# Optimization experiments

Hardware: AMD Instinct MI355X
Metric: run time of the kernel (lower is better)

The kernel has to match this reference:

```python
import jax, jax.numpy as jnp
import numpy as np

EPS = 1e-8  # torch.nn.functional.cosine_similarity default eps


def setup_inputs() -> dict:
    key = jax.random.key(0)
    k1, k2 = jax.random.split(key)
    P, B, D = 64, 512, 1024
    z_list = jax.random.normal(k1, (P, B, D), dtype=jnp.float32)
    z_avg = jax.random.normal(k2, (B, D), dtype=jnp.float32)  # passed but unused (overwritten in forward)
    return {"z_list": z_list, "z_avg": z_avg}


def reference(z_list, z_avg):
    # z_list: (P, B, D). The original overwrites z_avg with the patch mean.
    P, B, _ = z_list.shape
    z_avg = jnp.mean(z_list, axis=0)  # (B, D)

    # cosine_similarity(z_list[p,i], z_avg[j]) via normalize + batched matmul
    zn = z_list / jnp.maximum(jnp.linalg.norm(z_list, axis=-1, keepdims=True), EPS)
    an = z_avg / jnp.maximum(jnp.linalg.norm(z_avg, axis=-1, keepdims=True), EPS)
    cos_sim = jnp.einsum("pbd,cd->pbc", zn, an) - 1.0  # (P, B, B)

    mask = ~jnp.eye(B, dtype=bool)  # zero out diagonal (i == j)
    z_dissim = jnp.sum(cos_sim * mask[None, :, :])
    count = jnp.sum(mask) * P  # B*(B-1)*P
    return z_dissim / count
```

## Files before the change

kernel.cpp:

```cpp
#include <hip/hip_runtime.h>
#include <math.h>

constexpr int P = 64, B = 512, D = 1024;
constexpr int D4 = D / 4;
constexpr int WAVES = 4;
constexpr int PC = P / WAVES;
constexpr int TB = 32;
#define EPS 1e-8f

__device__ inline float wave_reduce_sum(float v) {
#pragma unroll
  for (int off = 1; off < 64; off <<= 1) v += __shfl_xor(v, off);
  return v;
}

__device__ inline float dot4(const float4& a, const float4& b) {
  return a.x * b.x + a.y * b.y + a.z * b.z + a.w * b.w;
}

__global__ __launch_bounds__(256) void k_main(const float* __restrict__ z,
                                              float* __restrict__ an,
                                              float* __restrict__ Uv,
                                              float* __restrict__ diag,
                                              float* __restrict__ out) {
  const int b = blockIdx.x;
  const int t = threadIdx.x;
  const int w = t >> 6;
  const int lane = t & 63;

  if (b == 0 && t == 0) out[0] = 0.f;

  __shared__ float4 lds_zs[WAVES][D4];
  __shared__ float4 lds_uu[WAVES][D4];
  __shared__ float red[2 * WAVES];

  float4 zs[4], uu[4];
#pragma unroll
  for (int k = 0; k < 4; ++k) {
    zs[k] = make_float4(0.f, 0.f, 0.f, 0.f);
    uu[k] = make_float4(0.f, 0.f, 0.f, 0.f);
  }

  const size_t pstride = (size_t)B * D4;
  const float4* base = (const float4*)z + ((size_t)(w * PC) * B + b) * D4;

  float4 curA[4], curB[4];
#pragma unroll
  for (int k = 0; k < 4; ++k) {
    curA[k] = base[k * 64 + lane];
    curB[k] = base[pstride + k * 64 + lane];
  }

  for (int pr = 0; pr < PC / 2; ++pr) {
    float4 nxtA[4], nxtB[4];
    const bool more = (pr + 1 < PC / 2);
    if (more) {
      const float4* nA = base + (size_t)(2 * pr + 2) * pstride;
      const float4* nB = base + (size_t)(2 * pr + 3) * pstride;
#pragma unroll
      for (int k = 0; k < 4; ++k) {
        nxtA[k] = nA[k * 64 + lane];
        nxtB[k] = nB[k * 64 + lane];
      }
    }

    float ssA = 0.f, ssB = 0.f;
#pragma unroll
    for (int k = 0; k < 4; ++k) {
      ssA += dot4(curA[k], curA[k]);
      ssB += dot4(curB[k], curB[k]);
    }
#pragma unroll
    for (int off = 1; off < 64; off <<= 1) {
      ssA += __shfl_xor(ssA, off);
      ssB += __shfl_xor(ssB, off);
    }
    const float wA = 1.0f / fmaxf(sqrtf(ssA), EPS);
    const float wB = 1.0f / fmaxf(sqrtf(ssB), EPS);

#pragma unroll
    for (int k = 0; k < 4; ++k) {
      zs[k].x += curA[k].x + curB[k].x;
      zs[k].y += curA[k].y + curB[k].y;
      zs[k].z += curA[k].z + curB[k].z;
      zs[k].w += curA[k].w + curB[k].w;
      uu[k].x += wA * curA[k].x + wB * curB[k].x;
      uu[k].y += wA * curA[k].y + wB * curB[k].y;
      uu[k].z += wA * curA[k].z + wB * curB[k].z;
      uu[k].w += wA * curA[k].w + wB * curB[k].w;
    }
    if (more) {
#pragma unroll
      for (int k = 0; k < 4; ++k) {
        curA[k] = nxtA[k];
        curB[k] = nxtB[k];
      }
    }
  }

#pragma unroll
  for (int k = 0; k < 4; ++k) {
    lds_zs[w][k * 64 + lane] = zs[k];
    lds_uu[w][k * 64 + lane] = uu[k];
  }
  __syncthreads();

  float4 zsum = make_float4(0.f, 0.f, 0.f, 0.f);
  float4 usum = make_float4(0.f, 0.f, 0.f, 0.f);
#pragma unroll
  for (int ww = 0; ww < WAVES; ++ww) {
    float4 a = lds_zs[ww][t];
    float4 u = lds_uu[ww][t];
    zsum.x += a.x; zsum.y += a.y; zsum.z += a.z; zsum.w += a.w;
    usum.x += u.x; usum.y += u.y; usum.z += u.z; usum.w += u.w;
  }

  float ss = dot4(zsum, zsum);
  ss = wave_reduce_sum(ss);
  if (lane == 0) red[w] = ss;
  __syncthreads();
  ss = red[0] + red[1] + red[2] + red[3];

  const float inv = 1.0f / fmaxf(sqrtf(ss), (float)P * EPS);
  float4 a4 = make_float4(zsum.x * inv, zsum.y * inv, zsum.z * inv, zsum.w * inv);

  ((float4*)an)[(size_t)b * D4 + t] = a4;
  ((float4*)Uv)[(size_t)b * D4 + t] = usum;

  float dg = dot4(usum, a4);
  dg = wave_reduce_sum(dg);
  if (lane == 0) red[WAVES + w] = dg;
  __syncthreads();
  if (t == 0) diag[b] = red[WAVES] + red[WAVES + 1] + red[WAVES + 2] + red[WAVES + 3];
}

__global__ __launch_bounds__(256) void k_tail(const float* __restrict__ an,
                                              const float* __restrict__ Uv,
                                              const float* __restrict__ diag,
                                              float* __restrict__ out) {
  const int blk = blockIdx.x;
  const int t = threadIdx.x;
  const int w = t >> 6;
  const int lane = t & 63;
  const int f4c = blk * 8 + (t & 7);
  const int rg = t >> 3;

  float4 S = make_float4(0.f, 0.f, 0.f, 0.f);
  float4 T = make_float4(0.f, 0.f, 0.f, 0.f);
#pragma unroll 4
  for (int i = 0; i < 16; ++i) {
    const size_t r = (size_t)rg + 32 * i;
    float4 a = ((const float4*)an)[r * D4 + f4c];
    float4 u = ((const float4*)Uv)[r * D4 + f4c];
    S.x += a.x; S.y += a.y; S.z += a.z; S.w += a.w;
    T.x += u.x; T.y += u.y; T.z += u.z; T.w += u.w;
  }

#pragma unroll
  for (int off = 8; off < 64; off <<= 1) {
    S.x += __shfl_xor(S.x, off); S.y += __shfl_xor(S.y, off);
    S.z += __shfl_xor(S.z, off); S.w += __shfl_xor(S.w, off);
    T.x += __shfl_xor(T.x, off); T.y += __shfl_xor(T.y, off);
    T.z += __shfl_xor(T.z, off); T.w += __shfl_xor(T.w, off);
  }

  __shared__ float4 ldsS[4][8], ldsT[4][8];
  if (lane < 8) {
    ldsS[w][lane] = S;
    ldsT[w][lane] = T;
  }
  __syncthreads();

  float dotp = 0.f;
  if (t < 8) {
    float4 Sf = ldsS[0][t], Tf = ldsT[0][t];
#pragma unroll
    for (int ww = 1; ww < 4; ++ww) {
      float4 s2 = ldsS[ww][t], t2 = ldsT[ww][t];
      Sf.x += s2.x; Sf.y += s2.y; Sf.z += s2.z; Sf.w += s2.w;
      Tf.x += t2.x; Tf.y += t2.y; Tf.z += t2.z; Tf.w += t2.w;
    }
    dotp = dot4(Sf, Tf);
  }
  float dgp = 0.f;
  if (t >= 16 && t < 32) dgp = diag[blk * 16 + (t - 16)];

  if (w == 0) {
    float v = dotp - dgp;
#pragma unroll
    for (int off = 1; off < 32; off <<= 1) v += __shfl_xor(v, off);
    if (t == 0) {
      const float count = 64.0f * 512.0f * 511.0f;
      float contrib = v / count + (blk == 0 ? -1.0f : 0.0f);
      atomicAdd(out, contrib);
    }
  }
}

extern "C" void kernel_launch(void* const* d_in, const int* in_sizes, int n_in,
                              void* d_out, int out_size, void* d_ws, size_t ws_size,
                              hipStream_t stream) {
  const float* z = (const float*)d_in[0];

  float* ws = (float*)d_ws;
  float* an = ws;
  float* Uv = an + (size_t)B * D;
  float* diag = Uv + (size_t)B * D;

  k_main<<<B, 256, 0, stream>>>(z, an, Uv, diag, (float*)d_out);
  k_tail<<<TB, 256, 0, stream>>>(an, Uv, diag, (float*)d_out);
}
```

Measured before the change: 31.97 us.

## Process two batch rows per block with contiguous 8 KB loads per patch

Each k_main block now handles two adjacent batch rows, so every patch step reads one contiguous 8 KB span (two rows) instead of two separate rows from different patches. The grid is halved to 256 blocks, and each thread keeps accumulators for both rows, which doubles register use. The goal is better memory coalescing and fewer blocks. In exchange, fewer blocks means fewer waves in flight to hide DRAM latency on a GPU with many CUs, and the epilogue reduction now runs twice per block with extra barriers.

```diff
diff --git a/kernel.cpp b/kernel.cpp
--- a/kernel.cpp
+++ b/kernel.cpp
@@ -23,52 +23,47 @@
                                               float* __restrict__ Uv,
                                               float* __restrict__ diag,
                                               float* __restrict__ out) {
-  const int b = blockIdx.x;
+  const int blk = blockIdx.x;
+  const int b0 = blk * 2;
   const int t = threadIdx.x;
   const int w = t >> 6;
   const int lane = t & 63;
 
-  if (b == 0 && t == 0) out[0] = 0.f;
+  if (blk == 0 && t == 0) out[0] = 0.f;
 
   __shared__ float4 lds_zs[WAVES][D4];
   __shared__ float4 lds_uu[WAVES][D4];
   __shared__ float red[2 * WAVES];
 
-  float4 zs[4], uu[4];
+  float4 zs0[4], uu0[4], zs1[4], uu1[4];
 #pragma unroll
   for (int k = 0; k < 4; ++k) {
-    zs[k] = make_float4(0.f, 0.f, 0.f, 0.f);
-    uu[k] = make_float4(0.f, 0.f, 0.f, 0.f);
+    zs0[k] = make_float4(0.f, 0.f, 0.f, 0.f);
+    uu0[k] = make_float4(0.f, 0.f, 0.f, 0.f);
+    zs1[k] = make_float4(0.f, 0.f, 0.f, 0.f);
+    uu1[k] = make_float4(0.f, 0.f, 0.f, 0.f);
   }
 
   const size_t pstride = (size_t)B * D4;
-  const float4* base = (const float4*)z + ((size_t)(w * PC) * B + b) * D4;
-
-  float4 curA[4], curB[4];
-#pragma unroll
-  for (int k = 0; k < 4; ++k) {
-    curA[k] = base[k * 64 + lane];
-    curB[k] = base[pstride + k * 64 + lane];
-  }
-
-  for (int pr = 0; pr < PC / 2; ++pr) {
-    float4 nxtA[4], nxtB[4];
-    const bool more = (pr + 1 < PC / 2);
+  const float4* base = (const float4*)z + ((size_t)(w * PC) * B + b0) * D4;
+
+  float4 cur[8], nxt[8];
+#pragma unroll
+  for (int k = 0; k < 8; ++k) cur[k] = base[k * 64 + lane];
+
+  for (int pp = 0; pp < PC; ++pp) {
+    const bool more = (pp + 1 < PC);
     if (more) {
-      const float4* nA = base + (size_t)(2 * pr + 2) * pstride;
-      const float4* nB = base + (size_t)(2 * pr + 3) * pstride;
-#pragma unroll
-      for (int k = 0; k < 4; ++k) {
-        nxtA[k] = nA[k * 64 + lane];
-        nxtB[k] = nB[k * 64 + lane];
-      }
+      const float4* nb = base + (size_t)(pp + 1) * pstride;
+#pragma unroll
+      for (int k = 0; k < 8; ++k) nxt[k] = nb[k * 64 + lane];
     }
 
     float ssA = 0.f, ssB = 0.f;
 #pragma unroll
     for (int k = 0; k < 4; ++k) {
-      ssA += dot4(curA[k], curA[k]);
-      ssB += dot4(curB[k], curB[k]);
+      ssA += dot4(cur[k], cur[k]);
+      ssB += dot4(cur[4 + k], cur[4 + k]);
     }
 #pragma unroll
     for (int off = 1; off < 64; off <<= 1) {
@@ -80,58 +75,57 @@
 
 #pragma unroll
     for (int k = 0; k < 4; ++k) {
-      zs[k].x += curA[k].x + curB[k].x;
-      zs[k].y += curA[k].y + curB[k].y;
-      zs[k].z += curA[k].z + curB[k].z;
-      zs[k].w += curA[k].w + curB[k].w;
-      uu[k].x += wA * curA[k].x + wB * curB[k].x;
-      uu[k].y += wA * curA[k].y + wB * curB[k].y;
-      uu[k].z += wA * curA[k].z + wB * curB[k].z;
-      uu[k].w += wA * curA[k].w + wB * curB[k].w;
+      const float4 a = cur[k], c = cur[4 + k];
+      zs0[k].x += a.x; zs0[k].y += a.y; zs0[k].z += a.z; zs0[k].w += a.w;
+      uu0[k].x += wA * a.x; uu0[k].y += wA * a.y;
+      uu0[k].z += wA * a.z; uu0[k].w += wA * a.w;
+      zs1[k].x += c.x; zs1[k].y += c.y; zs1[k].z += c.z; zs1[k].w += c.w;
+      uu1[k].x += wB * c.x; uu1[k].y += wB * c.y;
+      uu1[k].z += wB * c.z; uu1[k].w += wB * c.w;
     }
     if (more) {
 #pragma unroll
-      for (int k = 0; k < 4; ++k) {
-        curA[k] = nxtA[k];
-        curB[k] = nxtB[k];
-      }
-    }
-  }
-
-#pragma unroll
-  for (int k = 0; k < 4; ++k) {
-    lds_zs[w][k * 64 + lane] = zs[k];
-    lds_uu[w][k * 64 + lane] = uu[k];
-  }
-  __syncthreads();
-
-  float4 zsum = make_float4(0.f, 0.f, 0.f, 0.f);
-  float4 usum = make_float4(0.f, 0.f, 0.f, 0.f);
-#pragma unroll
-  for (int ww = 0; ww < WAVES; ++ww) {
-    float4 a = lds_zs[ww][t];
-    float4 u = lds_uu[ww][t];
-    zsum.x += a.x; zsum.y += a.y; zsum.z += a.z; zsum.w += a.w;
-    usum.x += u.x; usum.y += u.y; usum.z += u.z; usum.w += u.w;
-  }
-
-  float ss = dot4(zsum, zsum);
-  ss = wave_reduce_sum(ss);
-  if (lane == 0) red[w] = ss;
-  __syncthreads();
-  ss = red[0] + red[1] + red[2] + red[3];
-
-  const float inv = 1.0f / fmaxf(sqrtf(ss), (float)P * EPS);
-  float4 a4 = make_float4(zsum.x * inv, zsum.y * inv, zsum.z * inv, zsum.w * inv);
-
-  ((float4*)an)[(size_t)b * D4 + t] = a4;
-  ((float4*)Uv)[(size_t)b * D4 + t] = usum;
-
-  float dg = dot4(usum, a4);
-  dg = wave_reduce_sum(dg);
-  if (lane == 0) red[WAVES + w] = dg;
-  __syncthreads();
-  if (t == 0) diag[b] = red[WAVES] + red[WAVES + 1] + red[WAVES + 2] + red[WAVES + 3];
+      for (int k = 0; k < 8; ++k) cur[k] = nxt[k];
+    }
+  }
+
+#pragma unroll
+  for (int bb = 0; bb < 2; ++bb) {
+    const int b = b0 + bb;
+#pragma unroll
+    for (int k = 0; k < 4; ++k) {
+      lds_zs[w][k * 64 + lane] = bb ? zs1[k] : zs0[k];
+      lds_uu[w][k * 64 + lane] = bb ? uu1[k] : uu0[k];
+    }
+    __syncthreads();
+
+    float4 zsum = make_float4(0.f, 0.f, 0.f, 0.f);
+    float4 usum = make_float4(0.f, 0.f, 0.f, 0.f);
+#pragma unroll
+    for (int ww = 0; ww < WAVES; ++ww) {
+      float4 a = lds_zs[ww][t];
+      float4 u = lds_uu[ww][t];
+      zsum.x += a.x; zsum.y += a.y; zsum.z += a.z; zsum.w += a.w;
+      usum.x += u.x; usum.y += u.y; usum.z += u.z; usum.w += u.w;
+    }
+
+    float ss = wave_reduce_sum(dot4(zsum, zsum));
+    if (lane == 0) red[w] = ss;
+    __syncthreads();
+    ss = red[0] + red[1] + red[2] + red[3];
+
+    const float inv = 1.0f / fmaxf(sqrtf(ss), (float)P * EPS);
+    float4 a4 = make_float4(zsum.x * inv, zsum.y * inv, zsum.z * inv, zsum.w * inv);
+
+    ((float4*)an)[(size_t)b * D4 + t] = a4;
+    ((float4*)Uv)[(size_t)b * D4 + t] = usum;
+
+    float dg = wave_reduce_sum(dot4(usum, a4));
+    if (lane == 0) red[WAVES + w] = dg;
+    __syncthreads();
+    if (t == 0) diag[b] = red[WAVES] + red[WAVES + 1] + red[WAVES + 2] + red[WAVES + 3];
+    __syncthreads();
+  }
 }
 
 __global__ __launch_bounds__(256) void k_tail(const float* __restrict__ an,
@@ -207,6 +201,6 @@
   float* Uv = an + (size_t)B * D;
   float* diag = Uv + (size_t)B * D;
 
-  k_main<<<B, 256, 0, stream>>>(z, an, Uv, diag, (float*)d_out);
+  k_main<<<B / 2, 256, 0, stream>>>(z, an, Uv, diag, (float*)d_out);
   k_tail<<<TB, 256, 0, stream>>>(an, Uv, diag, (float*)d_out);
 }
```

Result: slower. 32.88 us (+2.8%).
